# Optimization experiments

Hardware: AMD Instinct MI355X
Metric: run time of the kernel (lower is better)

Reference implementation:

```python
import jax, jax.numpy as jnp
import numpy as np

N_GENE, N_DRUG, N_CLASS, N_FAM = 100000, 50000, 2000, 5000
D = 64
E_CG, E_CP, E_GF = 2000000, 100000, 200000
N_PAIRS = 100000


def setup_inputs() -> dict:
    key = jax.random.key(0)
    ks = jax.random.split(key, 32)
    nrm = lambda k, s, sc=0.1: jax.random.normal(k, s, jnp.float32) * sc
    ri = lambda k, n, hi: jax.random.randint(k, (n,), 0, hi, jnp.int32)
    inp = {
        "gene_emb": nrm(ks[0], (N_GENE, D)),
        "drug_emb": nrm(ks[1], (N_DRUG, D)),
        "class_emb": nrm(ks[2], (N_CLASS, D)),
        "family_emb": nrm(ks[3], (N_FAM, D)),
        "W_msg": nrm(ks[4], (2, 6, D, D)),
        "b_msg": jnp.zeros((2, 6, D), jnp.float32),
        "W_root": nrm(ks[5], (2, 6, D, D)),
        "Wc1": nrm(ks[6], (2 * D, D)),
        "bc1": jnp.zeros((D,), jnp.float32),
        "Wc2": nrm(ks[7], (D, 4)),
        "bc2": jnp.zeros((4,), jnp.float32),
        "e_cg_src": ri(ks[8], E_CG, N_DRUG), "e_cg_dst": ri(ks[9], E_CG, N_GENE),
        "e_gc_src": ri(ks[10], E_CG, N_GENE), "e_gc_dst": ri(ks[11], E_CG, N_DRUG),
        "e_cp_src": ri(ks[12], E_CP, N_DRUG), "e_cp_dst": ri(ks[13], E_CP, N_CLASS),
        "e_pc_src": ri(ks[14], E_CP, N_CLASS), "e_pc_dst": ri(ks[15], E_CP, N_DRUG),
        "e_gf_src": ri(ks[16], E_GF, N_GENE), "e_gf_dst": ri(ks[17], E_GF, N_FAM),
        "e_fg_src": ri(ks[18], E_GF, N_FAM), "e_fg_dst": ri(ks[19], E_GF, N_GENE),
        "pair_drug": ri(ks[20], N_PAIRS, N_DRUG),
        "pair_gene": ri(ks[21], N_PAIRS, N_GENE),
    }
    return inp


def _sage(x_src, x_dst, src, dst, n_dst, Wm, bm, Wr):
    # PyG SAGEConv(aggr='mean'): lin_l(mean_j x_src[j]) + lin_r(x_dst)
    msg = x_src[src]                                            # [E, D] gather
    agg = jax.ops.segment_sum(msg, dst, num_segments=n_dst)     # [n_dst, D]
    cnt = jax.ops.segment_sum(jnp.ones(src.shape, msg.dtype), dst, num_segments=n_dst)
    mean = agg / jnp.maximum(cnt, 1.0)[:, None]                 # isolated nodes -> 0
    return mean @ Wm + bm + x_dst @ Wr


def reference(gene_emb, drug_emb, class_emb, family_emb, W_msg, b_msg, W_root,
              Wc1, bc1, Wc2, bc2,
              e_cg_src, e_cg_dst, e_gc_src, e_gc_dst, e_cp_src, e_cp_dst,
              e_pc_src, e_pc_dst, e_gf_src, e_gf_dst, e_fg_src, e_fg_dst,
              pair_drug, pair_gene):
    sizes = {"gene": N_GENE, "compound": N_DRUG, "pclass": N_CLASS, "family": N_FAM}
    rels = [  # (src_type, dst_type, src_idx, dst_idx), order matches W_msg relation axis
        ("compound", "gene", e_cg_src, e_cg_dst),
        ("gene", "compound", e_gc_src, e_gc_dst),
        ("compound", "pclass", e_cp_src, e_cp_dst),
        ("pclass", "compound", e_pc_src, e_pc_dst),
        ("gene", "family", e_gf_src, e_gf_dst),
        ("family", "gene", e_fg_src, e_fg_dst),
    ]
    x = {"gene": gene_emb, "compound": drug_emb, "pclass": class_emb, "family": family_emb}
    num_layers = 2
    for l in range(num_layers):
        out = {k: jnp.zeros((sizes[k], D), jnp.float32) for k in sizes}  # HeteroConv aggr='sum'
        for r, (s, d, src, dst) in enumerate(rels):
            out[d] = out[d] + _sage(x[s], x[d], src, dst, sizes[d],
                                    W_msg[l, r], b_msg[l, r], W_root[l, r])
        x = out
        if l < num_layers - 1:
            x = {k: jax.nn.relu(v) for k, v in x.items()}  # dropout = identity (eval)
    h = jnp.concatenate([x["compound"][pair_drug], x["gene"][pair_gene]], axis=-1)  # [N, 2D]
    h = jax.nn.relu(h @ Wc1 + bc1)
    return h @ Wc2 + bc2  # [N, 4]
```

## Files before the change

kernel.cpp:

```cpp
#include <hip/hip_runtime.h>
#include <hip/hip_bf16.h>

#define NG 100000
#define ND 50000
#define NC 2000
#define NF 5000
#define DD 64

#define BSH 9
#define BINW 512
#define NREL 6
#define NB_CG ((NG + BINW - 1) / BINW)
#define NB_GC ((ND + BINW - 1) / BINW)
#define NB_CP ((NC + BINW - 1) / BINW)
#define NB_PC ((ND + BINW - 1) / BINW)
#define NB_GF ((NF + BINW - 1) / BINW)
#define NB_FG ((NG + BINW - 1) / BINW)
#define TOTB (NB_CG + NB_GC + NB_CP + NB_PC + NB_GF + NB_FG)
#define CHUNK 4096

typedef _Float16 h2_t __attribute__((ext_vector_type(2)));
typedef _Float16 half8 __attribute__((ext_vector_type(8)));
typedef float f32x4 __attribute__((ext_vector_type(4)));
typedef float f32x2 __attribute__((ext_vector_type(2)));
typedef unsigned char uchar;

__device__ inline uint packh2_rne(float a, float b) {
    h2_t h; h.x = (_Float16)a; h.y = (_Float16)b;
    return __builtin_bit_cast(uint, h);
}
__device__ inline uint packh2(float a, float b) {
    return __builtin_bit_cast(uint, __builtin_amdgcn_cvt_pkrtz(a, b));
}
__device__ inline float2 h2f2(uint u) {
    h2_t h = __builtin_bit_cast(h2_t, u);
    return make_float2((float)h.x, (float)h.y);
}
__device__ inline float fdot2u(uint m, uint w, float acc) {
#if __has_builtin(__builtin_amdgcn_fdot2)
    return __builtin_amdgcn_fdot2(__builtin_bit_cast(h2_t, m),
                                  __builtin_bit_cast(h2_t, w), acc, false);
#else
    float2 a = h2f2(m), b = h2f2(w);
    return acc + a.x * b.x + a.y * b.y;
#endif
}

#if __has_builtin(__builtin_amdgcn_cvt_pk_f32_fp8) && __has_builtin(__builtin_amdgcn_cvt_pk_fp8_f32)
template <bool HI>
__device__ inline f32x2 dec_pk8(uint u) {
    return __builtin_amdgcn_cvt_pk_f32_fp8(u, HI);
}
__device__ inline uint enc2_fp8(float a, float b) {
    return __builtin_amdgcn_cvt_pk_fp8_f32(a, b, 0u, false) & 0xffffu;
}
__device__ inline uint enc1_fp8(float a) {
    return __builtin_amdgcn_cvt_pk_fp8_f32(a, a, 0u, false) & 0xffu;
}
#else
template <bool HI>
__device__ inline f32x2 dec_pk8(uint u) {
    uint pair = HI ? (u >> 16) : (u & 0xffffu);
    uint b0 = pair & 0xffu, b1 = (pair >> 8) & 0xffu;
    ushort h0 = (ushort)(((b0 & 0x80u) << 8) | ((b0 & 0x7fu) << 7));
    ushort h1 = (ushort)(((b1 & 0x80u) << 8) | ((b1 & 0x7fu) << 7));
    f32x2 r;
    r.x = 256.f * (float)__builtin_bit_cast(_Float16, h0);
    r.y = 256.f * (float)__builtin_bit_cast(_Float16, h1);
    return r;
}
__device__ inline uint enc1_fp8(float x) {
    ushort h = __builtin_bit_cast(ushort, (_Float16)(x * 0.00390625f));
    uint mag = h & 0x7fffu;
    uint r = (mag + 0x3fu + ((mag >> 7) & 1u)) >> 7;
    if (r > 0x7eu) r = 0x7eu;
    return r | ((h >> 8) & 0x80u);
}
__device__ inline uint enc2_fp8(float a, float b) {
    return enc1_fp8(a) | (enc1_fp8(b) << 8);
}
#endif

struct Cvt4 { const float* in[4]; uint* out[4]; ushort* out8[4]; int n2[4]; };
struct EdgeJobs {
    const int* src[NREL]; const int* dst[NREL];
    int binbase[NREL]; int E[NREL]; int blk_end[NREL];
};
struct BPackJobs {
    const float* A[6]; const float* B[6]; const float* Ra[6]; const float* Rb[6];
    uint4* out[6]; int nkt[6];
};

struct MegaA {
    EdgeJobs ej; Cvt4 cv; BPackJobs bp;
    const float* Wc1; uint2* pwWc1;
    int hist_blocks, cvt_blocks;
    int* ghist;
};
__global__ __launch_bounds__(256) void megaA_kernel(MegaA a) {
    int b = blockIdx.x;
    if (b < a.hist_blocks) {
        __shared__ int lh[TOTB];
        for (int t = threadIdx.x; t < TOTB; t += 256) lh[t] = 0;
        __syncthreads();
        int j = 0;
        while (b >= a.ej.blk_end[j]) ++j;
        int b0 = j ? a.ej.blk_end[j - 1] : 0;
        int e0 = (b - b0) * CHUNK;
        const int* dst = a.ej.dst[j];
        int E = a.ej.E[j], bb = a.ej.binbase[j];
        for (int t = threadIdx.x; t < CHUNK; t += 256) {
            int e = e0 + t;
            if (e < E) atomicAdd(&lh[bb + (dst[e] >> BSH)], 1);
        }
        __syncthreads();
        for (int t = threadIdx.x; t < TOTB; t += 256)
            if (lh[t]) atomicAdd(&a.ghist[t], lh[t]);
    } else if (b < a.hist_blocks + a.cvt_blocks) {
        int cb = b - a.hist_blocks;
        for (int j = 0; j < 4; ++j) {
            int n2 = a.cv.n2[j];
            const float2* ip = (const float2*)a.cv.in[j];
            uint* op = a.cv.out[j];
            ushort* o8 = a.cv.out8[j];
            for (int i = cb * 256 + threadIdx.x; i < n2; i += a.cvt_blocks * 256) {
                float2 v = ip[i];
                op[i] = packh2_rne(v.x, v.y);
                if (o8) o8[i] = (ushort)enc2_fp8(v.x, v.y);
            }
        }
    } else if (b == a.hist_blocks + a.cvt_blocks) {
        const float* A = a.Wc1;
        uint2* o = a.pwWc1;
        for (int t = threadIdx.x; t < 32 * 64; t += 256) {
            int k4 = t >> 6, c = t & 63;
            float v0 = A[(4 * k4 + 0) * 64 + c];
            float v1 = A[(4 * k4 + 1) * 64 + c];
            float v2 = A[(4 * k4 + 2) * 64 + c];
            float v3 = A[(4 * k4 + 3) * 64 + c];
            o[t] = make_uint2(packh2_rne(v0, v1), packh2_rne(v2, v3));
        }
    } else {
        int pj = b - a.hist_blocks - a.cvt_blocks - 1;
        const float* A = a.bp.A[pj];
        const float* B = a.bp.B[pj];
        const float* Ra = a.bp.Ra[pj];
        const float* Rb = a.bp.Rb[pj];
        uint4* o = a.bp.out[pj];
        int n = a.bp.nkt[pj] * 4 * 64;
        for (int t = threadIdx.x; t < n; t += 256) {
            int kt = t >> 8, nt = (t >> 6) & 3, l = t & 63;
            int col = nt * 16 + (l & 15);
            float v[8];
#pragma unroll
            for (int j = 0; j < 8; ++j) {
                int k = kt * 32 + ((l >> 4) << 3) + j;
                int sel = k >> 6, r = k & 63;
                float x;
                if (sel == 0) x = A[r * 64 + col];
                else if (sel == 1 && B) x = B[r * 64 + col];
                else x = Ra[r * 64 + col] + (Rb ? Rb[r * 64 + col] : 0.f);
                v[j] = x;
            }
            o[t] = make_uint4(packh2_rne(v[0], v[1]), packh2_rne(v[2], v[3]),
                              packh2_rne(v[4], v[5]), packh2_rne(v[6], v[7]));
        }
    }
}

__global__ void scanB_kernel(const int* __restrict__ ghist, int* __restrict__ gbinstart,
                             int* __restrict__ gcursor) {
    int lane = threadIdx.x;
    if (lane >= 64) return;
    int carry = 0;
    for (int base = 0; base < TOTB; base += 64) {
        int idx = base + lane;
        int v = (idx < TOTB) ? ghist[idx] : 0;
        int ts = v;
        for (int d = 1; d < 64; d <<= 1) { int t = __shfl_up(ts, d); if (lane >= d) ts += t; }
        int excl = carry + ts - v;
        if (idx < TOTB) { gbinstart[idx] = excl; gcursor[idx] = excl; }
        carry += __shfl(ts, 63);
    }
    if (lane == 0) gbinstart[TOTB] = carry;
}

__global__ __launch_bounds__(256) void scatC_kernel(EdgeJobs ej, int* __restrict__ gcursor,
                                                    int* __restrict__ binned) {
    __shared__ int lh[TOTB], lbase[TOTB];
    for (int t = threadIdx.x; t < TOTB; t += 256) lh[t] = 0;
    __syncthreads();
    int b = blockIdx.x, j = 0;
    while (b >= ej.blk_end[j]) ++j;
    int b0 = j ? ej.blk_end[j - 1] : 0;
    int e0 = (b - b0) * CHUNK;
    const int* dst = ej.dst[j];
    const int* srcp = ej.src[j];
    int E = ej.E[j], bb = ej.binbase[j];
    for (int t = threadIdx.x; t < CHUNK; t += 256) {
        int e = e0 + t;
        if (e < E) atomicAdd(&lh[bb + (dst[e] >> BSH)], 1);
    }
    __syncthreads();
    for (int t = threadIdx.x; t < TOTB; t += 256) {
        int c = lh[t];
        if (c) { lbase[t] = atomicAdd(&gcursor[t], c); lh[t] = 0; }
    }
    __syncthreads();
    for (int t = threadIdx.x; t < CHUNK; t += 256) {
        int e = e0 + t;
        if (e < E) {
            int d = dst[e];
            int bin = bb + (d >> BSH);
            int p = atomicAdd(&lh[bin], 1);
            binned[lbase[bin] + p] = (srcp[e] << BSH) | (d & (BINW - 1));
        }
    }
}

struct BinMeta { int relbase[NREL + 1]; int* off[NREL]; int ndst[NREL]; };
__global__ __launch_bounds__(256) void csrD_kernel(BinMeta bmt, const int* __restrict__ gbinstart,
                                                   const int* __restrict__ binned,
                                                   int* __restrict__ adj) {
    __shared__ int lcnt[BINW], lexc[BINW];
    int b = blockIdx.x, j = 0;
    while (b >= bmt.relbase[j + 1]) ++j;
    int lb = b - bmt.relbase[j];
    int n0 = lb << BSH;
    int nn = bmt.ndst[j] - n0; if (nn > BINW) nn = BINW;
    int es = gbinstart[b], ee = gbinstart[b + 1];
    for (int t = threadIdx.x; t < BINW; t += 256) lcnt[t] = 0;
    __syncthreads();
    for (int t = es + threadIdx.x; t < ee; t += 256)
        atomicAdd(&lcnt[binned[t] & (BINW - 1)], 1);
    __syncthreads();
    if (threadIdx.x < 64) {
        int lane = threadIdx.x, carry = 0;
        for (int base = 0; base < BINW; base += 64) {
            int v = lcnt[base + lane];
            int ts = v;
            for (int d = 1; d < 64; d <<= 1) { int t2 = __shfl_up(ts, d); if (lane >= d) ts += t2; }
            lexc[base + lane] = carry + ts - v;
            carry += __shfl(ts, 63);
        }
    }
    __syncthreads();
    int* off = bmt.off[j];
    for (int t = threadIdx.x; t < nn; t += 256) off[n0 + t] = es + lexc[t];
    if (threadIdx.x == 0 && n0 + nn == bmt.ndst[j]) off[bmt.ndst[j]] = ee;
    for (int t = threadIdx.x; t < BINW; t += 256) lcnt[t] = 0;
    __syncthreads();
    for (int t = es + threadIdx.x; t < ee; t += 256) {
        int v = binned[t];
        int dl = v & (BINW - 1);
        int p = atomicAdd(&lcnt[dl], 1);
        adj[es + lexc[dl] + p] = v >> BSH;
    }
}

struct GJob { const int* off; const void* x; uint4* cat; int cstr, colbase, n, mode; };
struct GatherJobs { GJob jb[6]; int blk_end[6]; };

__global__ __launch_bounds__(256) void gather_kernel(GatherJobs g, const int* __restrict__ adj) {
    int b = blockIdx.x, j = 0;
    while (b >= g.blk_end[j]) ++j;
    int b0 = j ? g.blk_end[j - 1] : 0;
    int nbk = g.blk_end[j] - b0;
    GJob jb = g.jb[j];
    int tid = threadIdx.x, w = tid >> 6, lane = tid & 63;
    int cq = lane & 7, rg = lane >> 3;
    if (jb.mode == 0) {
        const uint2* x8 = (const uint2*)jb.x;
        int side = rg >> 2, sub = rg & 3;
        int npair = (jb.n + 1) >> 1;
        for (int p = (b - b0) * 4 + w; p < npair; p += nbk * 4) {
            int ia = p * 2;
            bool hb = (ia + 1 < jb.n);
            int a0 = jb.off[ia], a1 = jb.off[ia + 1];
            int b1 = hb ? jb.off[ia + 2] : a1;
            int cnt = side ? (b1 - a1) : (a1 - a0);
            const int* base = adj + (side ? a1 : a0);
            float s0 = 0, s1 = 0, s2 = 0, s3 = 0, s4 = 0, s5 = 0, s6 = 0, s7 = 0;
            int full = cnt & ~3;
            for (int e = sub; e < full; e += 4) {
                uint2 v = x8[(long long)base[e] * 8 + cq];
                f32x2 p01 = dec_pk8<false>(v.x), p23 = dec_pk8<true>(v.x);
                f32x2 p45 = dec_pk8<false>(v.y), p67 = dec_pk8<true>(v.y);
                s0 += p01.x; s1 += p01.y; s2 += p23.x; s3 += p23.y;
                s4 += p45.x; s5 += p45.y; s6 += p67.x; s7 += p67.y;
            }
            int e = full + sub;
            if (e < cnt) {
                uint2 v = x8[(long long)base[e] * 8 + cq];
                f32x2 p01 = dec_pk8<false>(v.x), p23 = dec_pk8<true>(v.x);
                f32x2 p45 = dec_pk8<false>(v.y), p67 = dec_pk8<true>(v.y);
                s0 += p01.x; s1 += p01.y; s2 += p23.x; s3 += p23.y;
                s4 += p45.x; s5 += p45.y; s6 += p67.x; s7 += p67.y;
            }
            s0 += __shfl_xor(s0, 8);  s1 += __shfl_xor(s1, 8);
            s2 += __shfl_xor(s2, 8);  s3 += __shfl_xor(s3, 8);
            s4 += __shfl_xor(s4, 8);  s5 += __shfl_xor(s5, 8);
            s6 += __shfl_xor(s6, 8);  s7 += __shfl_xor(s7, 8);
            s0 += __shfl_xor(s0, 16); s1 += __shfl_xor(s1, 16);
            s2 += __shfl_xor(s2, 16); s3 += __shfl_xor(s3, 16);
            s4 += __shfl_xor(s4, 16); s5 += __shfl_xor(s5, 16);
            s6 += __shfl_xor(s6, 16); s7 += __shfl_xor(s7, 16);
            float invf = 1.f / fmaxf((float)cnt, 1.f);
            if (sub == 0 && (side == 0 || hb)) {
                int node = ia + side;
                uint4 o = make_uint4(packh2(s0 * invf, s1 * invf), packh2(s2 * invf, s3 * invf),
                                     packh2(s4 * invf, s5 * invf), packh2(s6 * invf, s7 * invf));
                jb.cat[(long long)node * jb.cstr + jb.colbase + cq] = o;
            }
        }
    } else {
        const uint4* x16 = (const uint4*)jb.x;
        for (int gp = (b - b0) * 4 + w; gp * 8 < jb.n; gp += nbk * 4) {
            int node = gp * 8 + rg;
            int nc = node < jb.n ? node : jb.n - 1;
            int o0 = jb.off[nc], o1 = jb.off[nc + 1];
            int cnt = (node < jb.n) ? (o1 - o0) : 0;
            half8 acc = {0, 0, 0, 0, 0, 0, 0, 0};
            for (int t = 0; t < cnt; ++t) {
                int idx = adj[o0 + t];
                acc += __builtin_bit_cast(half8, x16[(long long)idx * 8 + cq]);
            }
            float invf = 1.f / fmaxf((float)cnt, 1.f);
            _Float16 ih = (_Float16)invf;
            half8 iv = {ih, ih, ih, ih, ih, ih, ih, ih};
            acc *= iv;
            if (node < jb.n)
                jb.cat[(long long)node * jb.cstr + jb.colbase + cq] =
                    __builtin_bit_cast(uint4, acc);
        }
    }
}

struct ApplyJobs {
    const uint4* cat[4]; const uint4* xr[4]; const uint4* Bimg[4];
    const float* bA[4]; const float* bB[4];
    ushort* out[4]; uchar* out8[4];
    int cat_kt[4]; int cstr4[4]; int n[4]; int relu[4]; int blk_end[4];
};
__global__ __launch_bounds__(256) void apply_kernel(ApplyJobs a, int njobs) {
    int b = blockIdx.x, j = 0;
    while (b >= a.blk_end[j]) ++j;
    int b0 = j ? a.blk_end[j - 1] : 0;
    int jb = a.blk_end[j] - b0;
    int n = a.n[j], cat_kt = a.cat_kt[j], cstr4 = a.cstr4[j], relu = a.relu[j];
    int K_kt = cat_kt + 2;
    const uint4* cat = a.cat[j];
    const uint4* xr = a.xr[j];
    const uint4* Bimg = a.Bimg[j];
    const float* bA = a.bA[j];
    const float* bB = a.bB[j];
    ushort* out = a.out[j];
    uchar* out8 = a.out8[j];
    int tid = threadIdx.x;
    int w = tid >> 6, lane = tid & 63;
    int mrow = lane & 15, koct = lane >> 4;
    int tiles = (n + 15) >> 4;
    for (int t = (b - b0) * 4 + w; t < tiles; t += jb * 4) {
        int m0 = t << 4;
        int row = m0 + mrow;
        if (row > n - 1) row = n - 1;
        f32x4 acc0 = {0.f, 0.f, 0.f, 0.f};
        f32x4 acc1 = {0.f, 0.f, 0.f, 0.f};
        f32x4 acc2 = {0.f, 0.f, 0.f, 0.f};
        f32x4 acc3 = {0.f, 0.f, 0.f, 0.f};
        for (int kt = 0; kt < K_kt; ++kt) {
            uint4 av;
            if (kt < cat_kt) av = cat[(long long)row * cstr4 + kt * 4 + koct];
            else av = xr[(long long)row * 8 + (kt - cat_kt) * 4 + koct];
            half8 af = __builtin_bit_cast(half8, av);
            const uint4* bp = Bimg + kt * 256 + lane;
            half8 b0f = __builtin_bit_cast(half8, bp[0]);
            half8 b1f = __builtin_bit_cast(half8, bp[64]);
            half8 b2f = __builtin_bit_cast(half8, bp[128]);
            half8 b3f = __builtin_bit_cast(half8, bp[192]);
            acc0 = __builtin_amdgcn_mfma_f32_16x16x32_f16(af, b0f, acc0, 0, 0, 0);
            acc1 = __builtin_amdgcn_mfma_f32_16x16x32_f16(af, b1f, acc1, 0, 0, 0);
            acc2 = __builtin_amdgcn_mfma_f32_16x16x32_f16(af, b2f, acc2, 0, 0, 0);
            acc3 = __builtin_amdgcn_mfma_f32_16x16x32_f16(af, b3f, acc3, 0, 0, 0);
        }
        int c = lane & 15, r0 = m0 + (lane >> 4) * 4;
        f32x4 accs[4] = {acc0, acc1, acc2, acc3};
#pragma unroll
        for (int nt = 0; nt < 4; ++nt) {
            int col = nt * 16 + c;
            float bias = bA[col] + (bB ? bB[col] : 0.f);
#pragma unroll
            for (int r = 0; r < 4; ++r) {
                int rw = r0 + r;
                if (rw < n) {
                    float v = accs[nt][r] + bias;
                    if (relu) v = fmaxf(v, 0.f);
                    if (out) out[(long long)rw * 64 + col] =
                        __builtin_bit_cast(ushort, (_Float16)v);
                    if (out8) out8[(long long)rw * 64 + col] = (uchar)enc1_fp8(v);
                }
            }
        }
    }
}

__global__ __launch_bounds__(256) void classifier_kernel(
        const ushort* __restrict__ xc, const ushort* __restrict__ xg,
        const int* __restrict__ pd, const int* __restrict__ pg,
        const uint2* __restrict__ gW1, const float* __restrict__ bc1,
        const float* __restrict__ Wc2, const float* __restrict__ bc2,
        float* __restrict__ out, int n) {
    __shared__ uint2 sW1[2048];
    __shared__ float sW2[256];
    __shared__ uint2 shp[4][32];
    __shared__ float sh1[4][65];
    int tid = threadIdx.x;
    for (int t = tid; t < 2048; t += 256) sW1[t] = gW1[t];
    if (tid < 256) sW2[tid] = Wc2[tid];
    __syncthreads();
    int lane = tid & 63, sub = tid >> 6;
    float b1 = bc1[lane];
    const uint* xcp = (const uint*)xc;
    const uint* xgp = (const uint*)xg;
    for (int base = blockIdx.x * 4; base < n; base += gridDim.x * 4) {
        int p = base + sub;
        if (p >= n) continue;
        int dp = pd[p], gp = pg[p];
        uint v = (lane < 32) ? xcp[(long long)dp * 32 + lane]
                             : xgp[(long long)gp * 32 + (lane - 32)];
        ((uint*)&shp[sub][0])[lane] = v;
        float acc = b1;
#pragma unroll
        for (int k4 = 0; k4 < 32; ++k4) {
            uint2 wv = sW1[k4 * 64 + lane];
            uint2 mv = shp[sub][k4];
            acc = fdot2u(mv.x, wv.x, acc);
            acc = fdot2u(mv.y, wv.y, acc);
        }
        sh1[sub][lane] = fmaxf(acc, 0.f);
        if (lane < 4) {
            float a2 = bc2[lane];
#pragma unroll 16
            for (int k = 0; k < 64; ++k) a2 += sh1[sub][k] * sW2[k * 4 + lane];
            out[(long long)p * 4 + lane] = a2;
        }
    }
}

extern "C" void kernel_launch(void* const* d_in, const int* in_sizes, int n_in,
                              void* d_out, int out_size, void* d_ws, size_t ws_size,
                              hipStream_t stream) {
    const float* gene = (const float*)d_in[0];
    const float* drug = (const float*)d_in[1];
    const float* pcls = (const float*)d_in[2];
    const float* famb = (const float*)d_in[3];
    const float* Wm   = (const float*)d_in[4];
    const float* bm   = (const float*)d_in[5];
    const float* Wr   = (const float*)d_in[6];
    const float* Wc1  = (const float*)d_in[7];
    const float* bc1  = (const float*)d_in[8];
    const float* Wc2  = (const float*)d_in[9];
    const float* bc2  = (const float*)d_in[10];
    const int* ecg_s = (const int*)d_in[11];
    const int* ecg_d = (const int*)d_in[12];
    const int* egc_s = (const int*)d_in[13];
    const int* egc_d = (const int*)d_in[14];
    const int* ecp_s = (const int*)d_in[15];
    const int* ecp_d = (const int*)d_in[16];
    const int* epc_s = (const int*)d_in[17];
    const int* epc_d = (const int*)d_in[18];
    const int* egf_s = (const int*)d_in[19];
    const int* egf_d = (const int*)d_in[20];
    const int* efg_s = (const int*)d_in[21];
    const int* efg_d = (const int*)d_in[22];
    const int* pair_d = (const int*)d_in[23];
    const int* pair_g = (const int*)d_in[24];
    const int E_CG = in_sizes[11];
    const int E_CP = in_sizes[15];
    const int E_GF = in_sizes[19];
    const int N_PAIRS = in_sizes[23];
    const long long TOT_E = 2LL * E_CG + 2LL * E_CP + 2LL * E_GF;

    ushort* g16   = (ushort*)d_ws;
    ushort* d16   = g16   + (long long)NG * DD;
    ushort* p16   = d16   + (long long)ND * DD;
    ushort* f16b  = p16   + (long long)NC * DD;
    ushort* x1g16 = f16b  + (long long)NF * DD;
    ushort* x1c16 = x1g16 + (long long)NG * DD;
    ushort* x1p16 = x1c16 + (long long)ND * DD;
    ushort* x1f16 = x1p16 + (long long)NC * DD;
    ushort* x2g16 = g16;
    ushort* x2c16 = d16;
    uint2* pwWc1 = (uint2*)(x1f16 + (long long)NF * DD);
    uint4* bimg = (uint4*)(pwWc1 + 2048);
    int* ghist = (int*)(bimg + 6 * 1536);
    int* gbinstart = ghist + TOTB;
    int* gcursor = gbinstart + TOTB + 1;
    int* off_cg = gcursor + TOTB;
    int* off_gc = off_cg + NG + 1;
    int* off_cp = off_gc + ND + 1;
    int* off_pc = off_cp + NC + 1;
    int* off_gf = off_pc + ND + 1;
    int* off_fg = off_gf + NF + 1;
    long long binned_off = (long long)(off_fg + NG + 1 - (int*)d_ws);
    binned_off = (binned_off + 3) & ~3LL;
    int* binned = (int*)d_ws + binned_off;
    int* adj    = binned + TOT_E;
    uint4* cat_c = (uint4*)binned;
    uint4* cat_p = cat_c + (long long)ND * 16;
    uint4* cat_f = cat_p + (long long)NC * 8;
    uint4* cat_g = (uint4*)(adj + TOT_E);
    uchar* g8  = (uchar*)(cat_g + (long long)NG * 16);
    uchar* d8v = g8  + (long long)NG * DD;
    uchar* x1g8 = g8;
    uchar* x1c8 = d8v;

    auto WmLR = [&](int l, int r) { return Wm + (long long)(l * 6 + r) * DD * DD; };
    auto WrLR = [&](int l, int r) { return Wr + (long long)(l * 6 + r) * DD * DD; };
    auto bmLR = [&](int l, int r) { return bm + (long long)(l * 6 + r) * DD; };

    EdgeJobs ej;
    const int* srcs[NREL] = {ecg_s, egc_s, ecp_s, epc_s, egf_s, efg_s};
    const int* dsts[NREL] = {ecg_d, egc_d, ecp_d, epc_d, egf_d, efg_d};
    int Es[NREL] = {E_CG, E_CG, E_CP, E_CP, E_GF, E_GF};
    int bb[NREL] = {0, NB_CG, NB_CG + NB_GC, NB_CG + NB_GC + NB_CP,
                    NB_CG + NB_GC + NB_CP + NB_PC, NB_CG + NB_GC + NB_CP + NB_PC + NB_GF};
    int acc_blocks = 0;
    for (int j = 0; j < NREL; ++j) {
        ej.src[j] = srcs[j]; ej.dst[j] = dsts[j];
        ej.E[j] = Es[j]; ej.binbase[j] = bb[j];
        acc_blocks += (Es[j] + CHUNK - 1) / CHUNK;
        ej.blk_end[j] = acc_blocks;
    }
    const int THIST = acc_blocks;
    const int CVTB = 1024;

    (void)hipMemsetAsync(ghist, 0, TOTB * sizeof(int), stream);
    MegaA ma;
    ma.ej = ej;
    ma.cv.in[0] = gene; ma.cv.out[0] = (uint*)g16;  ma.cv.out8[0] = (ushort*)g8;  ma.cv.n2[0] = NG * DD / 2;
    ma.cv.in[1] = drug; ma.cv.out[1] = (uint*)d16;  ma.cv.out8[1] = (ushort*)d8v; ma.cv.n2[1] = ND * DD / 2;
    ma.cv.in[2] = pcls; ma.cv.out[2] = (uint*)p16;  ma.cv.out8[2] = nullptr;      ma.cv.n2[2] = NC * DD / 2;
    ma.cv.in[3] = famb; ma.cv.out[3] = (uint*)f16b; ma.cv.out8[3] = nullptr;      ma.cv.n2[3] = NF * DD / 2;
    ma.Wc1 = Wc1; ma.pwWc1 = pwWc1;
    auto setbp = [&](int j, const float* A, const float* B, const float* Ra, const float* Rb, int nkt) {
        ma.bp.A[j] = A; ma.bp.B[j] = B; ma.bp.Ra[j] = Ra; ma.bp.Rb[j] = Rb;
        ma.bp.out[j] = bimg + j * 1536; ma.bp.nkt[j] = nkt;
    };
    setbp(0, WmLR(0, 0), WmLR(0, 5), WrLR(0, 0), WrLR(0, 5), 6);
    setbp(1, WmLR(0, 1), WmLR(0, 3), WrLR(0, 1), WrLR(0, 3), 6);
    setbp(2, WmLR(0, 2), nullptr,    WrLR(0, 2), nullptr,    4);
    setbp(3, WmLR(0, 4), nullptr,    WrLR(0, 4), nullptr,    4);
    setbp(4, WmLR(1, 0), WmLR(1, 5), WrLR(1, 0), WrLR(1, 5), 6);
    setbp(5, WmLR(1, 1), WmLR(1, 3), WrLR(1, 1), WrLR(1, 3), 6);
    ma.hist_blocks = THIST; ma.cvt_blocks = CVTB;
    ma.ghist = ghist;
    megaA_kernel<<<THIST + CVTB + 1 + 6, 256, 0, stream>>>(ma);

    scanB_kernel<<<1, 64, 0, stream>>>(ghist, gbinstart, gcursor);
    scatC_kernel<<<THIST, 256, 0, stream>>>(ej, gcursor, binned);
    BinMeta bmt;
    int rb[NREL + 1] = {0, NB_CG, NB_CG + NB_GC, NB_CG + NB_GC + NB_CP,
                        NB_CG + NB_GC + NB_CP + NB_PC,
                        NB_CG + NB_GC + NB_CP + NB_PC + NB_GF, TOTB};
    int* offs[NREL] = {off_cg, off_gc, off_cp, off_pc, off_gf, off_fg};
    int nds[NREL] = {NG, ND, NC, ND, NF, NG};
    for (int j = 0; j <= NREL; ++j) bmt.relbase[j] = rb[j];
    for (int j = 0; j < NREL; ++j) { bmt.off[j] = offs[j]; bmt.ndst[j] = nds[j]; }
    csrD_kernel<<<TOTB, 256, 0, stream>>>(bmt, gbinstart, binned, adj);

    auto ablk = [](int n) { int b = ((n + 15) / 16 + 3) / 4; return b > 1024 ? 1024 : b; };
    auto gb = [](int E) { int b = E / 1024; if (b < 8) b = 8; if (b > 2048) b = 2048; return b; };

    {
        GatherJobs g;
        int acc = 0;
        auto setg = [&](int j, const int* off, const void* x, uint4* cat,
                        int cstr, int colbase, int n, int mode, int E) {
            g.jb[j].off = off; g.jb[j].x = x; g.jb[j].cat = cat;
            g.jb[j].cstr = cstr; g.jb[j].colbase = colbase; g.jb[j].n = n; g.jb[j].mode = mode;
            acc += gb(E); g.blk_end[j] = acc;
        };
        setg(0, off_cg, d8v,  cat_g, 16, 0, NG, 0, E_CG);
        setg(1, off_fg, f16b, cat_g, 16, 8, NG, 1, E_GF);
        setg(2, off_gc, g8,   cat_c, 16, 0, ND, 0, E_CG);
        setg(3, off_pc, p16,  cat_c, 16, 8, ND, 1, E_CP);
        setg(4, off_cp, d8v,  cat_p, 8, 0, NC, 0, E_CP);
        setg(5, off_gf, g8,   cat_f, 8, 0, NF, 0, E_GF);
        gather_kernel<<<acc, 256, 0, stream>>>(g, adj);

        ApplyJobs ap;
        auto seta = [&](int j, const uint4* cat, int ckt, int cstr4, const ushort* xr,
                        const uint4* Bi, const float* biA, const float* biB,
                        ushort* out, uchar* out8, int n, int relu) {
            ap.cat[j] = cat; ap.cat_kt[j] = ckt; ap.cstr4[j] = cstr4;
            ap.xr[j] = (const uint4*)xr; ap.Bimg[j] = Bi; ap.bA[j] = biA; ap.bB[j] = biB;
            ap.out[j] = out; ap.out8[j] = out8; ap.n[j] = n; ap.relu[j] = relu;
        };
        seta(0, cat_g, 4, 16, g16,  bimg + 0 * 1536, bmLR(0, 0), bmLR(0, 5), x1g16, x1g8, NG, 1);
        seta(1, cat_c, 4, 16, d16,  bimg + 1 * 1536, bmLR(0, 1), bmLR(0, 3), x1c16, x1c8, ND, 1);
        seta(2, cat_p, 2, 8,  p16,  bimg + 2 * 1536, bmLR(0, 2), nullptr,    x1p16, nullptr, NC, 1);
        seta(3, cat_f, 2, 8,  f16b, bimg + 3 * 1536, bmLR(0, 4), nullptr,    x1f16, nullptr, NF, 1);
        int acc2 = 0;
        for (int j = 0; j < 4; ++j) { acc2 += ablk(ap.n[j]); ap.blk_end[j] = acc2; }
        apply_kernel<<<acc2, 256, 0, stream>>>(ap, 4);
    }

    {
        GatherJobs g;
        int acc = 0;
        auto setg = [&](int j, const int* off, const void* x, uint4* cat,
                        int cstr, int colbase, int n, int mode, int E) {
            g.jb[j].off = off; g.jb[j].x = x; g.jb[j].cat = cat;
            g.jb[j].cstr = cstr; g.jb[j].colbase = colbase; g.jb[j].n = n; g.jb[j].mode = mode;
            acc += gb(E); g.blk_end[j] = acc;
        };
        setg(0, off_cg, x1c8,  cat_g, 16, 0, NG, 0, E_CG);
        setg(1, off_fg, x1f16, cat_g, 16, 8, NG, 1, E_GF);
        setg(2, off_gc, x1g8,  cat_c, 16, 0, ND, 0, E_CG);
        setg(3, off_pc, x1p16, cat_c, 16, 8, ND, 1, E_CP);
        g.jb[4] = g.jb[3]; g.jb[4].n = 0; g.blk_end[4] = acc;
        g.jb[5] = g.jb[3]; g.jb[5].n = 0; g.blk_end[5] = acc;
        gather_kernel<<<acc, 256, 0, stream>>>(g, adj);

        ApplyJobs ap;
        ap.cat[0] = cat_g; ap.cat_kt[0] = 4; ap.cstr4[0] = 16;
        ap.xr[0] = (const uint4*)x1g16; ap.Bimg[0] = bimg + 4 * 1536;
        ap.bA[0] = bmLR(1, 0); ap.bB[0] = bmLR(1, 5);
        ap.out[0] = x2g16; ap.out8[0] = nullptr; ap.n[0] = NG; ap.relu[0] = 0;
        ap.cat[1] = cat_c; ap.cat_kt[1] = 4; ap.cstr4[1] = 16;
        ap.xr[1] = (const uint4*)x1c16; ap.Bimg[1] = bimg + 5 * 1536;
        ap.bA[1] = bmLR(1, 1); ap.bB[1] = bmLR(1, 3);
        ap.out[1] = x2c16; ap.out8[1] = nullptr; ap.n[1] = ND; ap.relu[1] = 0;
        for (int j = 2; j < 4; ++j) {
            ap.cat[j] = nullptr; ap.xr[j] = nullptr; ap.Bimg[j] = nullptr;
            ap.bA[j] = nullptr; ap.bB[j] = nullptr; ap.out[j] = nullptr; ap.out8[j] = nullptr;
            ap.n[j] = 0; ap.relu[j] = 0; ap.cat_kt[j] = 2; ap.cstr4[j] = 8;
        }
        int acc2 = ablk(NG); ap.blk_end[0] = acc2; acc2 += ablk(ND); ap.blk_end[1] = acc2;
        ap.blk_end[2] = acc2; ap.blk_end[3] = acc2;
        apply_kernel<<<acc2, 256, 0, stream>>>(ap, 2);
    }

    int cblocks = (N_PAIRS + 3) / 4;
    if (cblocks > 2048) cblocks = 2048;
    classifier_kernel<<<cblocks, 256, 0, stream>>>(x2c16, x2g16, pair_d, pair_g,
                                                   pwWc1, bc1, Wc2, bc2,
                                                   (float*)d_out, N_PAIRS);
}
```

Measured before the change: 486.0 us.

## Partition gather jobs across XCD groups and unroll neighbor loads

Replaces the linear block-to-job mapping in the gather kernel with a fixed 1024-block grid. Blocks are assigned by XCD (blockIdx & 7), so each half of the XCDs serves a different subset of relations. The intent is to keep each source-embedding table resident in the L2 caches of fewer XCDs and to balance work with hand-tuned slot splits. The mode-0 inner loop is also unrolled to issue four independent index and feature loads before accumulating, which raises memory-level parallelism at the cost of clamped redundant loads on tails.

```diff
diff --git a/kernel.cpp b/kernel.cpp
--- a/kernel.cpp
+++ b/kernel.cpp
@@ -18,6 +18,7 @@
 #define NB_FG ((NG + BINW - 1) / BINW)
 #define TOTB (NB_CG + NB_GC + NB_CP + NB_PC + NB_GF + NB_FG)
 #define CHUNK 4096
+#define NSLOT 128
 
 typedef _Float16 h2_t __attribute__((ext_vector_type(2)));
 typedef _Float16 half8 __attribute__((ext_vector_type(8)));
@@ -259,63 +260,80 @@
 }
 
 struct GJob { const int* off; const void* x; uint4* cat; int cstr, colbase, n, mode; };
-struct GatherJobs { GJob jb[6]; int blk_end[6]; };
-
-__global__ __launch_bounds__(256) void gather_kernel(GatherJobs g, const int* __restrict__ adj) {
-    int b = blockIdx.x, j = 0;
-    while (b >= g.blk_end[j]) ++j;
-    int b0 = j ? g.blk_end[j - 1] : 0;
-    int nbk = g.blk_end[j] - b0;
+struct GSched {
+    GJob jb[6];
+    int gjobs[2][4];
+    int gend[2][4];
+};
+
+__device__ inline void acc8(uint2 v, float* s) {
+    f32x2 p01 = dec_pk8<false>(v.x), p23 = dec_pk8<true>(v.x);
+    f32x2 p45 = dec_pk8<false>(v.y), p67 = dec_pk8<true>(v.y);
+    s[0] += p01.x; s[1] += p01.y; s[2] += p23.x; s[3] += p23.y;
+    s[4] += p45.x; s[5] += p45.y; s[6] += p67.x; s[7] += p67.y;
+}
+
+__global__ __launch_bounds__(256) void gather_kernel(GSched g, const int* __restrict__ adj) {
+    int b = blockIdx.x;
+    int xcd = b & 7, slot = b >> 3;
+    int grp = xcd >> 2;
+    int k = 0;
+    while (k < 3 && slot >= g.gend[grp][k]) ++k;
+    int j = g.gjobs[grp][k];
+    if (j < 0) return;
+    int s0 = k ? g.gend[grp][k - 1] : 0;
+    int W = 4 * (g.gend[grp][k] - s0);
+    int worker = (xcd & 3) + 4 * (slot - s0);
     GJob jb = g.jb[j];
     int tid = threadIdx.x, w = tid >> 6, lane = tid & 63;
     int cq = lane & 7, rg = lane >> 3;
+    int start = worker * 4 + w, stride = W * 4;
     if (jb.mode == 0) {
         const uint2* x8 = (const uint2*)jb.x;
         int side = rg >> 2, sub = rg & 3;
         int npair = (jb.n + 1) >> 1;
-        for (int p = (b - b0) * 4 + w; p < npair; p += nbk * 4) {
+        for (int p = start; p < npair; p += stride) {
             int ia = p * 2;
             bool hb = (ia + 1 < jb.n);
             int a0 = jb.off[ia], a1 = jb.off[ia + 1];
             int b1 = hb ? jb.off[ia + 2] : a1;
             int cnt = side ? (b1 - a1) : (a1 - a0);
             const int* base = adj + (side ? a1 : a0);
-            float s0 = 0, s1 = 0, s2 = 0, s3 = 0, s4 = 0, s5 = 0, s6 = 0, s7 = 0;
-            int full = cnt & ~3;
-            for (int e = sub; e < full; e += 4) {
-                uint2 v = x8[(long long)base[e] * 8 + cq];
-                f32x2 p01 = dec_pk8<false>(v.x), p23 = dec_pk8<true>(v.x);
-                f32x2 p45 = dec_pk8<false>(v.y), p67 = dec_pk8<true>(v.y);
-                s0 += p01.x; s1 += p01.y; s2 += p23.x; s3 += p23.y;
-                s4 += p45.x; s5 += p45.y; s6 += p67.x; s7 += p67.y;
+            float s[8] = {0, 0, 0, 0, 0, 0, 0, 0};
+            int l = cnt - 1;
+            for (int jj = 0; jj < cnt; jj += 16) {
+                int e0 = jj + sub, e1 = e0 + 4, e2 = e0 + 8, e3 = e0 + 12;
+                int i0 = base[e0 < l ? e0 : l];
+                int i1 = base[e1 < l ? e1 : l];
+                int i2 = base[e2 < l ? e2 : l];
+                int i3 = base[e3 < l ? e3 : l];
+                uint2 v0 = x8[(long long)i0 * 8 + cq];
+                uint2 v1 = x8[(long long)i1 * 8 + cq];
+                uint2 v2 = x8[(long long)i2 * 8 + cq];
+                uint2 v3 = x8[(long long)i3 * 8 + cq];
+                if (e0 < cnt) acc8(v0, s);
+                if (e1 < cnt) acc8(v1, s);
+                if (e2 < cnt) acc8(v2, s);
+                if (e3 < cnt) acc8(v3, s);
             }
-            int e = full + sub;
-            if (e < cnt) {
-                uint2 v = x8[(long long)base[e] * 8 + cq];
-                f32x2 p01 = dec_pk8<false>(v.x), p23 = dec_pk8<true>(v.x);
-                f32x2 p45 = dec_pk8<false>(v.y), p67 = dec_pk8<true>(v.y);
-                s0 += p01.x; s1 += p01.y; s2 += p23.x; s3 += p23.y;
-                s4 += p45.x; s5 += p45.y; s6 += p67.x; s7 += p67.y;
+#pragma unroll
+            for (int q = 0; q < 8; ++q) {
+                s[q] += __shfl_xor(s[q], 8);
+                s[q] += __shfl_xor(s[q], 16);
             }
-            s0 += __shfl_xor(s0, 8);  s1 += __shfl_xor(s1, 8);
-            s2 += __shfl_xor(s2, 8);  s3 += __shfl_xor(s3, 8);
-            s4 += __shfl_xor(s4, 8);  s5 += __shfl_xor(s5, 8);
-            s6 += __shfl_xor(s6, 8);  s7 += __shfl_xor(s7, 8);
-            s0 += __shfl_xor(s0, 16); s1 += __shfl_xor(s1, 16);
-            s2 += __shfl_xor(s2, 16); s3 += __shfl_xor(s3, 16);
-            s4 += __shfl_xor(s4, 16); s5 += __shfl_xor(s5, 16);
-            s6 += __shfl_xor(s6, 16); s7 += __shfl_xor(s7, 16);
             float invf = 1.f / fmaxf((float)cnt, 1.f);
             if (sub == 0 && (side == 0 || hb)) {
                 int node = ia + side;
-                uint4 o = make_uint4(packh2(s0 * invf, s1 * invf), packh2(s2 * invf, s3 * invf),
-                                     packh2(s4 * invf, s5 * invf), packh2(s6 * invf, s7 * invf));
+                uint4 o = make_uint4(packh2(s[0] * invf, s[1] * invf),
+                                     packh2(s[2] * invf, s[3] * invf),
+                                     packh2(s[4] * invf, s[5] * invf),
+                                     packh2(s[6] * invf, s[7] * invf));
                 jb.cat[(long long)node * jb.cstr + jb.colbase + cq] = o;
             }
         }
     } else {
         const uint4* x16 = (const uint4*)jb.x;
-        for (int gp = (b - b0) * 4 + w; gp * 8 < jb.n; gp += nbk * 4) {
+        for (int gp = start; gp * 8 < jb.n; gp += stride) {
             int node = gp * 8 + rg;
             int nc = node < jb.n ? node : jb.n - 1;
             int o0 = jb.off[nc], o1 = jb.off[nc + 1];
@@ -570,24 +588,27 @@
     csrD_kernel<<<TOTB, 256, 0, stream>>>(bmt, gbinstart, binned, adj);
 
     auto ablk = [](int n) { int b = ((n + 15) / 16 + 3) / 4; return b > 1024 ? 1024 : b; };
-    auto gb = [](int E) { int b = E / 1024; if (b < 8) b = 8; if (b > 2048) b = 2048; return b; };
+    auto setjb = [](GSched& g, int j, const int* off, const void* x, uint4* cat,
+                    int cstr, int colbase, int n, int mode) {
+        g.jb[j].off = off; g.jb[j].x = x; g.jb[j].cat = cat;
+        g.jb[j].cstr = cstr; g.jb[j].colbase = colbase; g.jb[j].n = n; g.jb[j].mode = mode;
+    };
 
     {
-        GatherJobs g;
-        int acc = 0;
-        auto setg = [&](int j, const int* off, const void* x, uint4* cat,
-                        int cstr, int colbase, int n, int mode, int E) {
-            g.jb[j].off = off; g.jb[j].x = x; g.jb[j].cat = cat;
-            g.jb[j].cstr = cstr; g.jb[j].colbase = colbase; g.jb[j].n = n; g.jb[j].mode = mode;
-            acc += gb(E); g.blk_end[j] = acc;
-        };
-        setg(0, off_cg, d8v,  cat_g, 16, 0, NG, 0, E_CG);
-        setg(1, off_fg, f16b, cat_g, 16, 8, NG, 1, E_GF);
-        setg(2, off_gc, g8,   cat_c, 16, 0, ND, 0, E_CG);
-        setg(3, off_pc, p16,  cat_c, 16, 8, ND, 1, E_CP);
-        setg(4, off_cp, d8v,  cat_p, 8, 0, NC, 0, E_CP);
-        setg(5, off_gf, g8,   cat_f, 8, 0, NF, 0, E_GF);
-        gather_kernel<<<acc, 256, 0, stream>>>(g, adj);
+        GSched g;
+        setjb(g, 0, off_cg, d8v,  cat_g, 16, 0, NG, 0);
+        setjb(g, 1, off_fg, f16b, cat_g, 16, 8, NG, 1);
+        setjb(g, 2, off_gc, g8,   cat_c, 16, 0, ND, 0);
+        setjb(g, 3, off_pc, p16,  cat_c, 16, 8, ND, 1);
+        setjb(g, 4, off_cp, d8v,  cat_p, 8, 0, NC, 0);
+        setjb(g, 5, off_gf, g8,   cat_f, 8, 0, NF, 0);
+        int ja[4] = {0, 4, 3, 1}, ea[4] = {106, 111, 116, NSLOT};
+        int jbv[4] = {2, 5, -1, -1}, ebv[4] = {116, NSLOT, NSLOT, NSLOT};
+        for (int q = 0; q < 4; ++q) {
+            g.gjobs[0][q] = ja[q]; g.gend[0][q] = ea[q];
+            g.gjobs[1][q] = jbv[q]; g.gend[1][q] = ebv[q];
+        }
+        gather_kernel<<<8 * NSLOT, 256, 0, stream>>>(g, adj);
 
         ApplyJobs ap;
         auto seta = [&](int j, const uint4* cat, int ckt, int cstr4, const ushort* xr,
@@ -607,21 +628,20 @@
     }
 
     {
-        GatherJobs g;
-        int acc = 0;
-        auto setg = [&](int j, const int* off, const void* x, uint4* cat,
-                        int cstr, int colbase, int n, int mode, int E) {
-            g.jb[j].off = off; g.jb[j].x = x; g.jb[j].cat = cat;
-            g.jb[j].cstr = cstr; g.jb[j].colbase = colbase; g.jb[j].n = n; g.jb[j].mode = mode;
-            acc += gb(E); g.blk_end[j] = acc;
-        };
-        setg(0, off_cg, x1c8,  cat_g, 16, 0, NG, 0, E_CG);
-        setg(1, off_fg, x1f16, cat_g, 16, 8, NG, 1, E_GF);
-        setg(2, off_gc, x1g8,  cat_c, 16, 0, ND, 0, E_CG);
-        setg(3, off_pc, x1p16, cat_c, 16, 8, ND, 1, E_CP);
-        g.jb[4] = g.jb[3]; g.jb[4].n = 0; g.blk_end[4] = acc;
-        g.jb[5] = g.jb[3]; g.jb[5].n = 0; g.blk_end[5] = acc;
-        gather_kernel<<<acc, 256, 0, stream>>>(g, adj);
+        GSched g;
+        setjb(g, 0, off_cg, x1c8,  cat_g, 16, 0, NG, 0);
+        setjb(g, 1, off_fg, x1f16, cat_g, 16, 8, NG, 1);
+        setjb(g, 2, off_gc, x1g8,  cat_c, 16, 0, ND, 0);
+        setjb(g, 3, off_pc, x1p16, cat_c, 16, 8, ND, 1);
+        setjb(g, 4, nullptr, nullptr, nullptr, 8, 0, 0, 0);
+        setjb(g, 5, nullptr, nullptr, nullptr, 8, 0, 0, 0);
+        int ja[4] = {0, 3, -1, -1}, ea[4] = {118, NSLOT, NSLOT, NSLOT};
+        int jbv[4] = {2, 1, -1, -1}, ebv[4] = {116, NSLOT, NSLOT, NSLOT};
+        for (int q = 0; q < 4; ++q) {
+            g.gjobs[0][q] = ja[q]; g.gend[0][q] = ea[q];
+            g.gjobs[1][q] = jbv[q]; g.gend[1][q] = ebv[q];
+        }
+        gather_kernel<<<8 * NSLOT, 256, 0, stream>>>(g, adj);
 
         ApplyJobs ap;
         ap.cat[0] = cat_g; ap.cat_kt[0] = 4; ap.cstr4[0] = 16;
```

New measurement: 614.6 us. +26.5%, slower.
